# Performance work log

Hardware: AMD Instinct MI355X
Metric: run time of the kernel (lower is better)

## Reference

```python
import jax, jax.numpy as jnp
import numpy as np

N = 4096      # n_patches / nodes
IN_FEAT = 512
EMBED = 512
HEADS = 8
HEAD_DIM = EMBED // HEADS
SCALING = HEAD_DIM ** -0.5


def setup_inputs() -> dict:
    key = jax.random.key(0)
    ks = jax.random.split(key, 7)
    x = jax.random.normal(ks[0], (N, IN_FEAT), dtype=jnp.float32)
    adj = jax.random.randint(ks[1], (N, N), 0, 2, dtype=jnp.int32)
    s = 0.04  # ~xavier scale for 512x512
    WQ = jax.random.normal(ks[2], (EMBED, IN_FEAT), dtype=jnp.float32) * s
    WK = jax.random.normal(ks[3], (EMBED, IN_FEAT), dtype=jnp.float32) * s
    WV = jax.random.normal(ks[4], (EMBED, IN_FEAT), dtype=jnp.float32) * s
    we = jax.random.normal(ks[5], (1, HEAD_DIM), dtype=jnp.float32) * 0.1
    be = jnp.zeros((1,), dtype=jnp.float32)
    return {"x": x, "adj": adj, "WQ": WQ, "WK": WK, "WV": WV, "we": we, "be": be}


def reference(x, adj, WQ, WK, WV, we, be):
    n = x.shape[0]
    # projections: [N, E] -> [H, N, head_dim]
    Q = (x @ WQ.T).reshape(n, HEADS, HEAD_DIM).transpose(1, 0, 2)
    K = (x @ WK.T).reshape(n, HEADS, HEAD_DIM).transpose(1, 0, 2)
    V = (x @ WV.T).reshape(n, HEADS, HEAD_DIM).transpose(1, 0, 2)
    # scores + per-query energy term: [H, N, N]
    energy = Q @ we.T + be                      # [H, N, 1]
    attn = jnp.einsum('hqd,hkd->hqk', Q, K) * SCALING + energy
    # adjacency mask (broadcast over heads)
    attn = attn + jnp.where(adj > 0, 0.0, -jnp.inf)
    attn = jax.nn.softmax(attn, axis=-1)
    # winner-take-all: one-hot at row max, divided by num_heads
    hard = (attn == jnp.max(attn, axis=-1, keepdims=True)).astype(jnp.float32) / HEADS
    out = jnp.einsum('hqk,hkd->hqd', hard, V)   # [H, N, head_dim]
    return out.transpose(1, 0, 2).reshape(n, EMBED)
```

## Files before the change

### kernel.cpp

```cpp
#include <hip/hip_runtime.h>
#include <hip/hip_bf16.h>
#include <float.h>
#include <stdint.h>

#define NPT    4096
#define EMB    512
#define NH     8
#define HD     64
#define KSPLIT 64

typedef __attribute__((ext_vector_type(8))) _Float16 f16x8;
typedef __attribute__((ext_vector_type(4))) float f32x4;
typedef __attribute__((ext_vector_type(16))) float f32x16;
typedef uint32_t u32;

#define LO_SCALE 2048.0f
#define LO_INV   4.8828125e-4f

__device__ __forceinline__ void async_ld16(const void* gsrc, void* ldst) {
    __builtin_amdgcn_global_load_lds(
        (const __attribute__((address_space(1))) u32*)gsrc,
        (__attribute__((address_space(3))) u32*)ldst, 16, 0, 0);
}

__device__ __forceinline__ void split2(float a, unsigned short& h, unsigned short& l) {
    _Float16 fh = (_Float16)a;
    float r = (a - (float)fh) * LO_SCALE;
    _Float16 fl = (_Float16)r;
    h = *reinterpret_cast<unsigned short*>(&fh);
    l = *reinterpret_cast<unsigned short*>(&fl);
}

__global__ __launch_bounds__(256) void prep_kernel(const float* __restrict__ x,
                                                   const float* __restrict__ wq,
                                                   const float* __restrict__ wk,
                                                   const float* __restrict__ wv,
                                                   const int* __restrict__ adj,
                                                   unsigned short* __restrict__ xs,
                                                   unsigned short* __restrict__ wqs,
                                                   unsigned short* __restrict__ wks,
                                                   unsigned short* __restrict__ wvs,
                                                   unsigned* __restrict__ bits_t) {
    int y = blockIdx.y;
    size_t i = (size_t)blockIdx.x * 256 + threadIdx.x;
    if (y == 4) {
        int q = (int)(i >> 7), w = (int)i & 127;
        const int4* p = (const int4*)(adj + (size_t)q * NPT + w * 32);
        unsigned m = 0;
#pragma unroll
        for (int j = 0; j < 8; ++j) {
            int4 v = p[j];
            m |= (v.x != 0 ? 1u : 0u) << (j * 4 + 0);
            m |= (v.y != 0 ? 1u : 0u) << (j * 4 + 1);
            m |= (v.z != 0 ? 1u : 0u) << (j * 4 + 2);
            m |= (v.w != 0 ? 1u : 0u) << (j * 4 + 3);
        }
        bits_t[(size_t)w * NPT + q] = m;
    } else if (y == 0) {
        const size_t PL = (size_t)NPT * EMB;
        float4 v = ((const float4*)x)[i];
        ushort4 h, l;
        split2(v.x, h.x, l.x);
        split2(v.y, h.y, l.y);
        split2(v.z, h.z, l.z);
        split2(v.w, h.w, l.w);
        ((ushort4*)xs)[i]        = h;
        ((ushort4*)(xs + PL))[i] = l;
    } else {
        const size_t WPL = 262144;
        if (i >= WPL / 4) return;
        const float* src = (y == 1) ? wq : (y == 2) ? wk : wv;
        unsigned short* dst = (y == 1) ? wqs : (y == 2) ? wks : wvs;
        float4 v = ((const float4*)src)[i];
        int e  = (int)(i >> 7);
        int k0 = ((int)i & 127) * 4;
        int ebk = e >> 6, el = e & 63;
        int kc = k0 >> 5, g = (k0 >> 3) & 3, dd = k0 & 7;
        size_t off = ((((size_t)ebk * 16 + kc) * 4 + g) * 64 + el) * 8 + dd;
        ushort4 h, l;
        split2(v.x, h.x, l.x);
        split2(v.y, h.y, l.y);
        split2(v.z, h.z, l.z);
        split2(v.w, h.w, l.w);
        *(ushort4*)(dst + off)       = h;
        *(ushort4*)(dst + WPL + off) = l;
    }
}

__global__ __launch_bounds__(256, 3) void gemm_mfma(const unsigned short* __restrict__ xs,
                                                    const unsigned short* __restrict__ wqs,
                                                    const unsigned short* __restrict__ wks,
                                                    const unsigned short* __restrict__ wvs,
                                                    unsigned short* __restrict__ Q2,
                                                    unsigned short* __restrict__ K2,
                                                    float* __restrict__ V) {
    const int z = blockIdx.z;
    const unsigned short* W2 = (z == 0) ? wqs : (z == 1) ? wks : wvs;
    const size_t XPL = (size_t)NPT * EMB;
    const size_t WPL = 262144;
    const size_t OPL = (size_t)NH * NPT * HD;

    const int nb = blockIdx.x * 128;
    const int ebk = blockIdx.y;
    const int tid = threadIdx.x;
    const int wvi = tid >> 6, lane = tid & 63;
    const int m = lane & 15, quad = lane >> 4;
    const int n0 = nb + wvi * 32;

    __shared__ __align__(16) unsigned short Ws[2][2 * 2048];

    auto prefetchW = [&](int kc, int buf) {
#pragma unroll
        for (int i2 = 0; i2 < 2; ++i2) {
            int c = wvi + 4 * i2;
            int p = c >> 2, sub = c & 3;
            const unsigned short* src = W2 + (size_t)p * WPL
                + ((size_t)ebk * 16 + kc) * 2048 + (sub * 64 + lane) * 8;
            async_ld16(src, &Ws[buf][p * 2048 + sub * 512]);
        }
    };
    f16x8 bfA[2][2], bfB[2][2];
    auto load_bf = [&](f16x8 (&bf)[2][2], int kc) {
#pragma unroll
        for (int nt = 0; nt < 2; ++nt)
#pragma unroll
            for (int p = 0; p < 2; ++p)
                bf[nt][p] = *(const f16x8*)(xs + (size_t)p * XPL
                    + (size_t)(n0 + nt * 16 + m) * EMB + kc * 32 + quad * 8);
    };

    f32x4 acc[2][4][2];
#pragma unroll
    for (int s = 0; s < 2; ++s)
#pragma unroll
        for (int mt = 0; mt < 4; ++mt)
#pragma unroll
            for (int nt = 0; nt < 2; ++nt) acc[s][mt][nt] = (f32x4){0.f, 0.f, 0.f, 0.f};

    prefetchW(0, 0);
    load_bf(bfA, 0);

    auto iter = [&](int kc, int buf, f16x8 (&cur)[2][2], f16x8 (&nxt)[2][2]) {
        asm volatile("s_waitcnt vmcnt(4)\n\ts_barrier" ::: "memory");
        if (kc < 15) { prefetchW(kc + 1, buf ^ 1); load_bf(nxt, kc + 1); }
#pragma unroll
        for (int ga = 0; ga < 2; ++ga) {
            f16x8 af[4];
#pragma unroll
            for (int mt = 0; mt < 4; ++mt)
                af[mt] = *(const f16x8*)&Ws[buf][ga * 2048 + (quad * 64 + mt * 16 + m) * 8];
#pragma unroll
            for (int pb = 0; pb < 2 - ga; ++pb)
#pragma unroll
                for (int mt = 0; mt < 4; ++mt)
#pragma unroll
                    for (int nt = 0; nt < 2; ++nt)
                        acc[ga + pb][mt][nt] = __builtin_amdgcn_mfma_f32_16x16x32_f16(
                            af[mt], cur[nt][pb], acc[ga + pb][mt][nt], 0, 0, 0);
        }
    };

#pragma unroll 1
    for (int kc2 = 0; kc2 < 16; kc2 += 2) {
        iter(kc2, 0, bfA, bfB);
        iter(kc2 + 1, 1, bfB, bfA);
    }

    const int h = ebk;
#pragma unroll
    for (int mt = 0; mt < 4; ++mt)
#pragma unroll
        for (int nt = 0; nt < 2; ++nt) {
            const int n = n0 + nt * 16 + m;
            const int d0 = mt * 16 + quad * 4;
            f32x4 a;
#pragma unroll
            for (int j = 0; j < 4; ++j)
                a[j] = fmaf(acc[1][mt][nt][j], LO_INV, acc[0][mt][nt][j]);
            if (z == 2) {
                *(f32x4*)(V + (size_t)n * EMB + ebk * 64 + d0) = a;
            } else {
                ushort4 ph, pl;
                split2(a[0], ph.x, pl.x);
                split2(a[1], ph.y, pl.y);
                split2(a[2], ph.z, pl.z);
                split2(a[3], ph.w, pl.w);
                unsigned short* O2 = (z == 0) ? Q2 : K2;
                size_t off = ((size_t)h * 128 + (n >> 5)) * 2048
                           + (d0 >> 3) * 256 + (n & 31) * 8 + (d0 & 7);
                *(ushort4*)(O2 + off)       = ph;
                *(ushort4*)(O2 + OPL + off) = pl;
            }
        }
}

__global__ __launch_bounds__(256, 4) void score_mfma(const unsigned short* __restrict__ Q2,
                                                     const unsigned short* __restrict__ K2,
                                                     const unsigned* __restrict__ bits_t,
                                                     float* __restrict__ pval,
                                                     int* __restrict__ pidx) {
    const int qb = blockIdx.x * 128;
    const int ks = blockIdx.y;
    const int tid = threadIdx.x;
    const int wvi = tid >> 6, lane = tid & 63;
    const int il = lane & 31, hi = lane >> 5;
    const size_t PL = (size_t)NH * NPT * HD;
    const int q0 = qb + wvi * 32;
    const int NT = NH * 2;

    __shared__ __align__(16) unsigned short Ks[3][2 * 2048 + 1024];

    auto prefetchK = [&](int t) {
        int h = t >> 1, kt = ks * 2 + (t & 1), buf = t % 3;
#pragma unroll
        for (int i2 = 0; i2 < 2; ++i2) {
            int c = wvi + 4 * i2;
            int p = c >> 2, sub = c & 3;
            const unsigned short* src = K2 + (size_t)p * PL
                + ((size_t)h * 128 + kt) * 2048 + (sub * 64 + lane) * 8;
            async_ld16(src, &Ks[buf][p * 2048 + sub * 512]);
        }
    };

    f16x8 qf[4][2];
    auto load_qf = [&](int hh) {
#pragma unroll
        for (int c = 0; c < 4; ++c)
#pragma unroll
            for (int p = 0; p < 2; ++p)
                qf[c][p] = *(const f16x8*)(Q2 + (size_t)p * PL
                    + ((size_t)hh * 128 + (q0 >> 5)) * 2048
                    + (c * 2 + hi) * 256 + il * 8);
    };

    load_qf(0);
    prefetchK(0);
    prefetchK(1);

    float bestv = -FLT_MAX; int besti = 0;

#pragma unroll 1
    for (int t = 0; t < NT; ++t) {
        const int h = t >> 1, kst = t & 1, buf = t % 3;
        const int kbase = ks * 64 + kst * 32;

        if (t + 1 < NT) asm volatile("s_waitcnt vmcnt(2)\n\ts_barrier" ::: "memory");
        else            asm volatile("s_waitcnt vmcnt(0)\n\ts_barrier" ::: "memory");

        if (kst == 0) { bestv = -FLT_MAX; besti = 0; }

        unsigned w = bits_t[(size_t)(ks * 2 + kst) * NPT + q0 + il];

        f32x16 acc0, acc1;
#pragma unroll
        for (int j = 0; j < 16; ++j) { acc0[j] = 0.f; acc1[j] = 0.f; }

        __builtin_amdgcn_s_setprio(1);
#pragma unroll
        for (int c = 0; c < 4; ++c) {
            f16x8 kfh = *(const f16x8*)&Ks[buf][(c * 2 + hi) * 256 + il * 8];
            f16x8 kfl = *(const f16x8*)&Ks[buf][2048 + (c * 2 + hi) * 256 + il * 8];
            acc0 = __builtin_amdgcn_mfma_f32_32x32x16_f16(kfh, qf[c][0], acc0, 0, 0, 0);
            acc1 = __builtin_amdgcn_mfma_f32_32x32x16_f16(kfh, qf[c][1], acc1, 0, 0, 0);
            acc1 = __builtin_amdgcn_mfma_f32_32x32x16_f16(kfl, qf[c][0], acc1, 0, 0, 0);
        }
        __builtin_amdgcn_s_setprio(0);

        if (kst == 1 && h + 1 < NH) load_qf(h + 1);
        if (t + 2 < NT) prefetchK(t + 2);

        const unsigned wsh = w >> (4 * hi);
        const int kbl = kbase + 4 * hi;
#pragma unroll
        for (int r = 0; r < 16; ++r) {
            float s = fmaf(acc1[r], LO_INV, acc0[r]);
            bool ok = (wsh >> ((r & 3) + 8 * (r >> 2))) & 1u;
            s = ok ? s : -FLT_MAX;
            int idx = kbl + (r & 3) + 8 * (r >> 2);
            bool g = s > bestv;
            bestv = g ? s : bestv;
            besti = g ? idx : besti;
        }

        if (kst == 1) {
            float v = bestv; int bi = besti;
            float ov = __shfl_xor(v, 32);
            int   oi = __shfl_xor(bi, 32);
            if (ov > v || (ov == v && oi < bi)) { v = ov; bi = oi; }
            if (hi == 0) {
                size_t o = ((size_t)h * KSPLIT + ks) * NPT + q0 + il;
                pval[o] = v; pidx[o] = bi;
            }
        }
    }
}

__global__ __launch_bounds__(256) void gather_out(const float* __restrict__ V,
                                                  const float* __restrict__ pval,
                                                  const int* __restrict__ pidx,
                                                  float* __restrict__ out) {
    const int q = blockIdx.x;
    const int tid = threadIdx.x;
    __shared__ int widx[NH];
    {
        const int h = tid >> 5, j = tid & 31;
        size_t o1 = ((size_t)h * KSPLIT + j) * NPT + q;
        size_t o2 = ((size_t)h * KSPLIT + j + 32) * NPT + q;
        float v1 = pval[o1]; int b1 = pidx[o1];
        float v2 = pval[o2]; int b2 = pidx[o2];
        bool t2 = (v2 > v1);
        float v = t2 ? v2 : v1; int bi = t2 ? b2 : b1;
#pragma unroll
        for (int o = 1; o < 32; o <<= 1) {
            float ov = __shfl_xor(v, o);
            int   oi = __shfl_xor(bi, o);
            if (ov > v || (ov == v && oi < bi)) { v = ov; bi = oi; }
        }
        if (j == 0) widx[h] = bi;
    }
    __syncthreads();
    if (tid < 128) {
        const int h = tid >> 4;
        const int d4 = (tid & 15) * 4;
        const int k = widx[h];
        float4 v = *(const float4*)(V + (size_t)k * EMB + h * HD + d4);
        v.x *= 0.125f; v.y *= 0.125f; v.z *= 0.125f; v.w *= 0.125f;
        *(float4*)(out + (size_t)q * EMB + h * HD + d4) = v;
    }
}

extern "C" void kernel_launch(void* const* d_in, const int* in_sizes, int n_in,
                              void* d_out, int out_size, void* d_ws, size_t ws_size,
                              hipStream_t stream) {
    const float* x   = (const float*)d_in[0];
    const int*   adj = (const int*)d_in[1];
    const float* WQ  = (const float*)d_in[2];
    const float* WK  = (const float*)d_in[3];
    const float* WV  = (const float*)d_in[4];
    float* out = (float*)d_out;

    char* ws = (char*)d_ws;
    const size_t HMB = 512u * 1024;
    unsigned short* xs   = (unsigned short*)(ws);
    unsigned short* wqs  = (unsigned short*)(ws + 16 * HMB);
    unsigned short* wks  = (unsigned short*)(ws + 18 * HMB);
    unsigned short* wvs  = (unsigned short*)(ws + 20 * HMB);
    unsigned short* Q2   = (unsigned short*)(ws + 32 * HMB);
    unsigned short* K2   = (unsigned short*)(ws + 48 * HMB);
    float*          V    = (float*)(ws + 64 * HMB);
    unsigned*       bits = (unsigned*)(ws + 80 * HMB);
    float*          pval = (float*)(ws);
    int*            pidx = (int*)(ws + 16 * HMB);

    prep_kernel<<<dim3(2048, 5), dim3(256), 0, stream>>>(x, WQ, WK, WV, adj,
                                                         xs, wqs, wks, wvs, bits);
    gemm_mfma<<<dim3(NPT / 128, NH, 3), dim3(256), 0, stream>>>(xs, wqs, wks, wvs, Q2, K2, V);
    score_mfma<<<dim3(NPT / 128, KSPLIT), dim3(256), 0, stream>>>(Q2, K2, bits, pval, pidx);
    gather_out<<<dim3(NPT), dim3(256), 0, stream>>>(V, pval, pidx, out);
}
```

Before: 250.2 us.

## Triple-buffer projection loads, remap score blocks per XCD, compact argmax index tracking

The projection GEMM moves from double to triple buffering of the W tiles in LDS and the x fragments in registers, keeping two k-chunks in flight, and fully unrolls the k loop. The score kernel remaps its block indices so blocks that share a K split land on the same XCD, aiming for better L2 reuse of K tiles. The inner argmax loop now tracks a compact code instead of the full index and rebuilds the index only at the end. The gather's tie-break becomes consistent with the lower-index rule. Risks are higher register and LDS use from the third buffer and the full unroll, which may reduce occupancy.

Measured after the change: 244.5 us. 2.3% less time.

```diff
diff --git a/kernel.cpp b/kernel.cpp
--- a/kernel.cpp
+++ b/kernel.cpp
@@ -107,7 +107,7 @@
     const int m = lane & 15, quad = lane >> 4;
     const int n0 = nb + wvi * 32;
 
-    __shared__ __align__(16) unsigned short Ws[2][2 * 2048];
+    __shared__ __align__(16) unsigned short Ws[3][2 * 2048];
 
     auto prefetchW = [&](int kc, int buf) {
 #pragma unroll
@@ -119,13 +119,13 @@
             async_ld16(src, &Ws[buf][p * 2048 + sub * 512]);
         }
     };
-    f16x8 bfA[2][2], bfB[2][2];
-    auto load_bf = [&](f16x8 (&bf)[2][2], int kc) {
+    f16x8 bf[3][2][2];
+    auto load_bf = [&](int set, int kc) {
 #pragma unroll
         for (int nt = 0; nt < 2; ++nt)
 #pragma unroll
             for (int p = 0; p < 2; ++p)
-                bf[nt][p] = *(const f16x8*)(xs + (size_t)p * XPL
+                bf[set][nt][p] = *(const f16x8*)(xs + (size_t)p * XPL
                     + (size_t)(n0 + nt * 16 + m) * EMB + kc * 32 + quad * 8);
     };
 
@@ -137,18 +137,23 @@
 #pragma unroll
             for (int nt = 0; nt < 2; ++nt) acc[s][mt][nt] = (f32x4){0.f, 0.f, 0.f, 0.f};
 
-    prefetchW(0, 0);
-    load_bf(bfA, 0);
-
-    auto iter = [&](int kc, int buf, f16x8 (&cur)[2][2], f16x8 (&nxt)[2][2]) {
-        asm volatile("s_waitcnt vmcnt(4)\n\ts_barrier" ::: "memory");
-        if (kc < 15) { prefetchW(kc + 1, buf ^ 1); load_bf(nxt, kc + 1); }
+    load_bf(0, 0); prefetchW(0, 0);
+    load_bf(1, 1); prefetchW(1, 1);
+
+#pragma unroll
+    for (int kc = 0; kc < 16; ++kc) {
+        if (kc == 15) asm volatile("s_waitcnt vmcnt(0)\n\ts_barrier" ::: "memory");
+        else          asm volatile("s_waitcnt vmcnt(6)\n\ts_barrier" ::: "memory");
+        if (kc + 2 < 16) {
+            load_bf((kc + 2) % 3, kc + 2);
+            prefetchW(kc + 2, (kc + 2) % 3);
+        }
 #pragma unroll
         for (int ga = 0; ga < 2; ++ga) {
             f16x8 af[4];
 #pragma unroll
             for (int mt = 0; mt < 4; ++mt)
-                af[mt] = *(const f16x8*)&Ws[buf][ga * 2048 + (quad * 64 + mt * 16 + m) * 8];
+                af[mt] = *(const f16x8*)&Ws[kc % 3][ga * 2048 + (quad * 64 + mt * 16 + m) * 8];
 #pragma unroll
             for (int pb = 0; pb < 2 - ga; ++pb)
 #pragma unroll
@@ -156,14 +161,8 @@
 #pragma unroll
                     for (int nt = 0; nt < 2; ++nt)
                         acc[ga + pb][mt][nt] = __builtin_amdgcn_mfma_f32_16x16x32_f16(
-                            af[mt], cur[nt][pb], acc[ga + pb][mt][nt], 0, 0, 0);
-        }
-    };
-
-#pragma unroll 1
-    for (int kc2 = 0; kc2 < 16; kc2 += 2) {
-        iter(kc2, 0, bfA, bfB);
-        iter(kc2 + 1, 1, bfB, bfA);
+                            af[mt], bf[kc % 3][nt][pb], acc[ga + pb][mt][nt], 0, 0, 0);
+        }
     }
 
     const int h = ebk;
@@ -199,8 +198,11 @@
                                                      const unsigned* __restrict__ bits_t,
                                                      float* __restrict__ pval,
                                                      int* __restrict__ pidx) {
-    const int qb = blockIdx.x * 128;
-    const int ks = blockIdx.y;
+    const int bid = blockIdx.x + 32 * blockIdx.y;
+    const int xcd = bid & 7, j = bid >> 3;
+    const int ks  = xcd * 8 + (j >> 5);
+    const int qb  = (j & 31) * 128;
+
     const int tid = threadIdx.x;
     const int wvi = tid >> 6, lane = tid & 63;
     const int il = lane & 31, hi = lane >> 5;
@@ -242,7 +244,6 @@
 #pragma unroll 1
     for (int t = 0; t < NT; ++t) {
         const int h = t >> 1, kst = t & 1, buf = t % 3;
-        const int kbase = ks * 64 + kst * 32;
 
         if (t + 1 < NT) asm volatile("s_waitcnt vmcnt(2)\n\ts_barrier" ::: "memory");
         else            asm volatile("s_waitcnt vmcnt(0)\n\ts_barrier" ::: "memory");
@@ -253,7 +254,7 @@
 
         f32x16 acc0, acc1;
 #pragma unroll
-        for (int j = 0; j < 16; ++j) { acc0[j] = 0.f; acc1[j] = 0.f; }
+        for (int j2 = 0; j2 < 16; ++j2) { acc0[j2] = 0.f; acc1[j2] = 0.f; }
 
         __builtin_amdgcn_s_setprio(1);
 #pragma unroll
@@ -270,20 +271,20 @@
         if (t + 2 < NT) prefetchK(t + 2);
 
         const unsigned wsh = w >> (4 * hi);
-        const int kbl = kbase + 4 * hi;
 #pragma unroll
         for (int r = 0; r < 16; ++r) {
             float s = fmaf(acc1[r], LO_INV, acc0[r]);
             bool ok = (wsh >> ((r & 3) + 8 * (r >> 2))) & 1u;
-            s = ok ? s : -FLT_MAX;
-            int idx = kbl + (r & 3) + 8 * (r >> 2);
-            bool g = s > bestv;
+            bool g = ok && (s > bestv);
             bestv = g ? s : bestv;
-            besti = g ? idx : besti;
+            besti = g ? (kst * 16 + r) : besti;
         }
 
         if (kst == 1) {
-            float v = bestv; int bi = besti;
+            int code = besti;
+            int bi = ks * 64 + ((code >> 4) << 5) + 4 * hi
+                   + (code & 3) + ((code >> 2) & 3) * 8;
+            float v = bestv;
             float ov = __shfl_xor(v, 32);
             int   oi = __shfl_xor(bi, 32);
             if (ov > v || (ov == v && oi < bi)) { v = ov; bi = oi; }
@@ -308,7 +309,7 @@
         size_t o2 = ((size_t)h * KSPLIT + j + 32) * NPT + q;
         float v1 = pval[o1]; int b1 = pidx[o1];
         float v2 = pval[o2]; int b2 = pidx[o2];
-        bool t2 = (v2 > v1);
+        bool t2 = (v2 > v1) || (v2 == v1 && b2 < b1);
         float v = t2 ? v2 : v1; int bi = t2 ? b2 : b1;
 #pragma unroll
         for (int o = 1; o < 32; o <<= 1) {
```
